# Performance work log

Hardware: AMD Instinct MI355X
Metric: run time of the kernel (lower is better)

The kernel has to match this reference:

```python
import jax, jax.numpy as jnp
import numpy as np

N = 100000      # nodes
E = 1600000     # edges
G = 8           # graphs in batch
H = 128         # hidden_dim
CNN = 768
MORPH = 6
NC = 5
EPS = 1e-5      # BatchNorm eps


def setup_inputs() -> dict:
    key = jax.random.key(0)
    ks = jax.random.split(key, 32)
    D = CNN + MORPH

    def w(k, shape, fan_in):
        # kaiming_normal_ (relu): std = sqrt(2/fan_in)
        return jax.random.normal(k, shape, jnp.float32) * np.sqrt(2.0 / fan_in)

    inp = {
        "cnn_features": jax.random.normal(ks[0], (N, CNN), jnp.float32),
        "morph_features": jax.random.normal(ks[1], (N, MORPH), jnp.float32),
        "cell_edge_index": jax.random.randint(ks[2], (2, E), 0, N, jnp.int32),
        "batch": jnp.sort(jax.random.randint(ks[3], (N,), 0, G, jnp.int32)),
        # GCN layers (weights stored [in, out])
        "gcn1_w": w(ks[4], (D, H), D), "gcn1_b": jnp.zeros((H,), jnp.float32),
        "gcn2_w": w(ks[5], (H, H), H), "gcn2_b": jnp.zeros((H,), jnp.float32),
        "gcn3_w": w(ks[6], (H, H), H), "gcn3_b": jnp.zeros((H,), jnp.float32),
        # BatchNorm affine params (eval mode, running_mean=0 running_var=1)
        "bn1_g": jnp.ones((H,), jnp.float32), "bn1_b": jnp.zeros((H,), jnp.float32),
        "bn2_g": jnp.ones((H,), jnp.float32), "bn2_b": jnp.zeros((H,), jnp.float32),
        "bn3_g": jnp.ones((H,), jnp.float32), "bn3_b": jnp.zeros((H,), jnp.float32),
        # attention gate: Linear(H,H) -> tanh -> Linear(H,1)
        "att_w1": w(ks[7], (H, H), H), "att_b1": jnp.zeros((H,), jnp.float32),
        "att_w2": w(ks[8], (H, 1), H), "att_b2": jnp.zeros((1,), jnp.float32),
        # classifier MLP
        "cls_w1": w(ks[9], (H, 2 * H), H), "cls_b1": jnp.zeros((2 * H,), jnp.float32),
        "cbn1_g": jnp.ones((2 * H,), jnp.float32), "cbn1_b": jnp.zeros((2 * H,), jnp.float32),
        "cls_w2": w(ks[10], (2 * H, H), 2 * H), "cls_b2": jnp.zeros((H,), jnp.float32),
        "cbn2_g": jnp.ones((H,), jnp.float32), "cbn2_b": jnp.zeros((H,), jnp.float32),
        "cls_w3": w(ks[11], (H, NC), H), "cls_b3": jnp.zeros((NC,), jnp.float32),
    }
    return inp


def _bn_eval(x, gamma, beta):
    # BatchNorm1d eval: running_mean=0, running_var=1
    return x * (gamma / np.sqrt(1.0 + EPS)) + beta


def _gcn(x, w, b, src, dst, dinv):
    h = x @ w                                   # [N, out]
    norm = dinv[src] * dinv[dst]                # [E]
    msg = h[src] * norm[:, None]                # [E, out]
    agg = jax.ops.segment_sum(msg, dst, num_segments=N)
    agg = agg + h * (dinv * dinv)[:, None]      # self-loop contribution
    return agg + b


def _forward(cnn_features, morph_features,
             gcn1_w, gcn1_b, gcn2_w, gcn2_b, gcn3_w, gcn3_b,
             bn1_g, bn1_b, bn2_g, bn2_b, bn3_g, bn3_b,
             att_w1, att_b1, att_w2, att_b2,
             cls_w1, cls_b1, cbn1_g, cbn1_b,
             cls_w2, cls_b2, cbn2_g, cbn2_b,
             cls_w3, cls_b3,
             cell_edge_index, batch):
    x = jnp.concatenate([cnn_features, morph_features], axis=1)  # [N, 774]
    src, dst = cell_edge_index[0], cell_edge_index[1]
    # symmetric GCN normalization with self-loops: deg = in-degree + 1
    deg = jax.ops.segment_sum(jnp.ones((E,), x.dtype), dst, num_segments=N) + 1.0
    dinv = jax.lax.rsqrt(deg)

    x1 = jax.nn.relu(_bn_eval(_gcn(x, gcn1_w, gcn1_b, src, dst, dinv), bn1_g, bn1_b))
    x2 = jax.nn.relu(_bn_eval(_gcn(x1, gcn2_w, gcn2_b, src, dst, dinv), bn2_g, bn2_b))
    x3 = jax.nn.relu(_bn_eval(_gcn(x2, gcn3_w, gcn3_b, src, dst, dinv), bn3_g, bn3_b))
    x_out = x1 + x2 + x3                                        # [N, H]

    # GlobalAttention pooling: segment softmax over per-graph nodes
    gate = jnp.tanh(x_out @ att_w1 + att_b1) @ att_w2 + att_b2  # [N, 1]
    gate = gate[:, 0]
    gmax = jax.ops.segment_max(gate, batch, num_segments=G)
    a = jnp.exp(gate - gmax[batch])
    denom = jax.ops.segment_sum(a, batch, num_segments=G)
    alpha = a / denom[batch]
    pooled = jax.ops.segment_sum(alpha[:, None] * x_out, batch, num_segments=G)  # [G, H]

    # classifier (dropout off, BN eval)
    h = jax.nn.relu(_bn_eval(pooled @ cls_w1 + cls_b1, cbn1_g, cbn1_b))
    h = jax.nn.relu(_bn_eval(h @ cls_w2 + cls_b2, cbn2_g, cbn2_b))
    return h @ cls_w3 + cls_b3                                  # [G, NC]


def reference(cnn_features, morph_features, cell_edge_index, batch,
              gcn1_w, gcn1_b, gcn2_w, gcn2_b, gcn3_w, gcn3_b,
              bn1_g, bn1_b, bn2_g, bn2_b, bn3_g, bn3_b,
              att_w1, att_b1, att_w2, att_b2,
              cls_w1, cls_b1, cbn1_g, cbn1_b,
              cls_w2, cls_b2, cbn2_g, cbn2_b,
              cls_w3, cls_b3):
    return _forward(cnn_features, morph_features,
                    gcn1_w, gcn1_b, gcn2_w, gcn2_b, gcn3_w, gcn3_b,
                    bn1_g, bn1_b, bn2_g, bn2_b, bn3_g, bn3_b,
                    att_w1, att_b1, att_w2, att_b2,
                    cls_w1, cls_b1, cbn1_g, cbn1_b,
                    cls_w2, cls_b2, cbn2_g, cbn2_b,
                    cls_w3, cls_b3,
                    cell_edge_index, batch)
```

## Files before the change

### kernel.cpp

```cpp
#include <hip/hip_runtime.h>
#include <hip/hip_bf16.h>

#define EPSV 1e-5f

typedef short short8v __attribute__((ext_vector_type(8)));
typedef float f32x4 __attribute__((ext_vector_type(4)));

__device__ __forceinline__ unsigned short f2bf(float f){
  unsigned u = __float_as_uint(f);
  unsigned r = u + 0x7fffu + ((u >> 16) & 1u);
  return (unsigned short)(r >> 16);
}
__device__ __forceinline__ unsigned pk2bf(float x, float y){
  return (unsigned)f2bf(x) | ((unsigned)f2bf(y) << 16);
}
__device__ __forceinline__ float bf2f(unsigned short s){
  return __uint_as_float(((unsigned)s) << 16);
}
__device__ __forceinline__ float bflo(unsigned u){ return __uint_as_float(u << 16); }
__device__ __forceinline__ float bfhi(unsigned u){ return __uint_as_float(u & 0xffff0000u); }

__global__ void hist_kernel(const int* __restrict__ dst, int* __restrict__ deg, int E){
  int i = blockIdx.x*256 + threadIdx.x;
  if (i < E) atomicAdd(&deg[dst[i]], 1);
}

__global__ void scan_partial(const int* __restrict__ deg, int* __restrict__ bsums, int N){
  __shared__ int sd[256];
  int t = threadIdx.x;
  int base = blockIdx.x*1024 + t*4;
  int s = 0;
  if (base+0 < N) s += deg[base+0];
  if (base+1 < N) s += deg[base+1];
  if (base+2 < N) s += deg[base+2];
  if (base+3 < N) s += deg[base+3];
  sd[t]=s; __syncthreads();
  for (int off=128; off>0; off>>=1){
    if (t<off) sd[t]+=sd[t+off];
    __syncthreads();
  }
  if (t==0) bsums[blockIdx.x]=sd[0];
}

__global__ void scan_bsums(int* bsums, int* row_start, int B, int N, int E){
  if (threadIdx.x==0 && blockIdx.x==0){
    int run=0;
    for (int b=0;b<B;b++){ int v=bsums[b]; bsums[b]=run; run+=v; }
    row_start[N]=E;
  }
}

__global__ void scan_final(const int* __restrict__ deg, const int* __restrict__ bsums,
                           int* __restrict__ row_start, int* __restrict__ cursor,
                           float* __restrict__ dinv, int N){
  __shared__ int sd[256];
  int t=threadIdx.x, b=blockIdx.x;
  int base=b*1024+t*4;
  int v0=0,v1=0,v2=0,v3=0;
  if (base+0<N) v0=deg[base+0];
  if (base+1<N) v1=deg[base+1];
  if (base+2<N) v2=deg[base+2];
  if (base+3<N) v3=deg[base+3];
  int s=v0+v1+v2+v3;
  sd[t]=s; __syncthreads();
  for (int off=1; off<256; off<<=1){
    int x = (t>=off)?sd[t-off]:0;
    __syncthreads();
    sd[t]+=x;
    __syncthreads();
  }
  int excl = sd[t]-s + bsums[b];
  int e0=excl, e1=excl+v0, e2=e1+v1, e3=e2+v2;
  if (base+0<N){ row_start[base+0]=e0; cursor[base+0]=e0; dinv[base+0]=rsqrtf((float)v0+1.0f); }
  if (base+1<N){ row_start[base+1]=e1; cursor[base+1]=e1; dinv[base+1]=rsqrtf((float)v1+1.0f); }
  if (base+2<N){ row_start[base+2]=e2; cursor[base+2]=e2; dinv[base+2]=rsqrtf((float)v2+1.0f); }
  if (base+3<N){ row_start[base+3]=e3; cursor[base+3]=e3; dinv[base+3]=rsqrtf((float)v3+1.0f); }
}

__global__ void scatter_kernel(const int* __restrict__ src, const int* __restrict__ dst,
                               int* __restrict__ cursor, int* __restrict__ csr_src, int E){
  int i = blockIdx.x*256 + threadIdx.x;
  if (i < E){
    int d = dst[i];
    int pos = atomicAdd(&cursor[d], 1);
    csr_src[pos] = src[i];
  }
}

__global__ void wsplit_kernel(const float* __restrict__ W, unsigned short* __restrict__ WT,
                              int D, int Dpad){
  int k = blockIdx.x*256 + threadIdx.x;
  int c = blockIdx.y;
  if (k >= Dpad) return;
  float v = (k < D) ? W[(size_t)k*128 + c] : 0.f;
  WT[(size_t)c*Dpad + k] = f2bf(v);
}

__global__ void wsplit_all(const float* __restrict__ W2, const float* __restrict__ W3,
                           const float* __restrict__ WA,
                           unsigned short* __restrict__ w2T, unsigned short* __restrict__ w3T,
                           unsigned short* __restrict__ aT_hi, unsigned short* __restrict__ aT_lo){
  int k = threadIdx.x;
  int c = blockIdx.y;
  int z = blockIdx.z;
  if (z == 0){
    w2T[c*128 + k] = f2bf(W2[(size_t)k*128 + c]);
  } else if (z == 1){
    w3T[c*128 + k] = f2bf(W3[(size_t)k*128 + c]);
  } else {
    float v = WA[(size_t)k*128 + c];
    unsigned short h = f2bf(v);
    aT_hi[c*128 + k] = h;
    aT_lo[c*128 + k] = f2bf(v - bf2f(h));
  }
}

#define LOADA(KC) { \
  const int gk0 = (KC) + akseg; \
  if ((Rst < N) && (gk0 + 32 <= Da)){ \
    const float4* p4 = (const float4*)(xa + (size_t)Rst*Da + gk0); \
    pa0=p4[0]; pa1=p4[1]; pa2=p4[2]; pa3=p4[3]; pa4=p4[4]; pa5=p4[5]; pa6=p4[6]; pa7=p4[7]; \
  } else { \
    float tmp[32]; \
    _Pragma("unroll") \
    for (int q=0;q<32;q++){ \
      int gk = gk0 + q; float x = 0.f; \
      if (Rst < N){ \
        if (gk < Da) x = xa[(size_t)Rst*Da + gk]; \
        else if (gk < D) x = xb[(size_t)Rst*Db + (gk - Da)]; \
      } \
      tmp[q]=x; } \
    pa0=*(float4*)&tmp[0];  pa1=*(float4*)&tmp[4];  pa2=*(float4*)&tmp[8];  pa3=*(float4*)&tmp[12]; \
    pa4=*(float4*)&tmp[16]; pa5=*(float4*)&tmp[20]; pa6=*(float4*)&tmp[24]; pa7=*(float4*)&tmp[28]; \
  } }

#define LOADW(KC) { \
  const unsigned short* ph = wrowp + (KC); \
  pw0=*(const uint4*)(ph); pw1=*(const uint4*)(ph+8); pw2=*(const uint4*)(ph+16); pw3=*(const uint4*)(ph+24); }

__global__ __launch_bounds__(256, 3) void gemm_mfma_kernel(
    const float* __restrict__ xa, const float* __restrict__ xb,
    const unsigned short* __restrict__ WT,
    unsigned short* __restrict__ outb, int N, int Da, int Db, int Dpad)
{
  __shared__ unsigned short Abf[128*64];
  __shared__ unsigned short Bbf[128*64];

  const int tid  = threadIdx.x;
  const int lane = tid & 63;
  const int wave = tid >> 6;
  const int lr   = lane & 15;
  const int kg   = lane >> 4;
  const int rowBase = blockIdx.x * 128;
  const int D = Da + Db;

  f32x4 acc[2][8];
  #pragma unroll
  for (int s=0;s<2;s++)
    #pragma unroll
    for (int c=0;c<8;c++){ acc[s][c][0]=0.f; acc[s][c][1]=0.f; acc[s][c][2]=0.f; acc[s][c][3]=0.f; }

  const int arow = tid >> 1;
  const int akseg = (tid & 1) * 32;
  const int Rst = rowBase + arow;
  const int abase = arow*128 + akseg*2;
  const int aswz  = (arow & 7) << 4;
  const unsigned short* wrowp = WT + (size_t)arow*Dpad + akseg;

  float4 pa0,pa1,pa2,pa3,pa4,pa5,pa6,pa7;
  uint4  pw0,pw1,pw2,pw3;

  LOADA(0)
  LOADW(0)

  for (int kc = 0; kc < Dpad; kc += 64){
    __syncthreads();
    {
      unsigned u[4];
      u[0]=pk2bf(pa0.x,pa0.y); u[1]=pk2bf(pa0.z,pa0.w); u[2]=pk2bf(pa1.x,pa1.y); u[3]=pk2bf(pa1.z,pa1.w);
      *(uint4*)((char*)Abf + ((abase+ 0)^aswz)) = *(const uint4*)u;
      u[0]=pk2bf(pa2.x,pa2.y); u[1]=pk2bf(pa2.z,pa2.w); u[2]=pk2bf(pa3.x,pa3.y); u[3]=pk2bf(pa3.z,pa3.w);
      *(uint4*)((char*)Abf + ((abase+16)^aswz)) = *(const uint4*)u;
      u[0]=pk2bf(pa4.x,pa4.y); u[1]=pk2bf(pa4.z,pa4.w); u[2]=pk2bf(pa5.x,pa5.y); u[3]=pk2bf(pa5.z,pa5.w);
      *(uint4*)((char*)Abf + ((abase+32)^aswz)) = *(const uint4*)u;
      u[0]=pk2bf(pa6.x,pa6.y); u[1]=pk2bf(pa6.z,pa6.w); u[2]=pk2bf(pa7.x,pa7.y); u[3]=pk2bf(pa7.z,pa7.w);
      *(uint4*)((char*)Abf + ((abase+48)^aswz)) = *(const uint4*)u;
      *(uint4*)((char*)Bbf + ((abase+ 0)^aswz)) = pw0;
      *(uint4*)((char*)Bbf + ((abase+16)^aswz)) = pw1;
      *(uint4*)((char*)Bbf + ((abase+32)^aswz)) = pw2;
      *(uint4*)((char*)Bbf + ((abase+48)^aswz)) = pw3;
    }
    __syncthreads();
    const int kn = kc + 64;
    if (kn < Dpad){
      LOADA(kn)
      LOADW(kn)
    }
    #pragma unroll
    for (int ks=0; ks<2; ks++){
      const int kb = ks*64 + kg*16;
      const int r0 = wave*32 + lr;
      const int r1 = r0 + 16;
      const int offA0 = (r0*128 + kb) ^ ((r0&7)<<4);
      const int offA1 = (r1*128 + kb) ^ ((r1&7)<<4);
      short8v a0 = *(const short8v*)((const char*)Abf + offA0);
      short8v a1 = *(const short8v*)((const char*)Abf + offA1);
      #pragma unroll
      for (int ct=0; ct<8; ct++){
        const int c = ct*16 + lr;
        const int offB = (c*128 + kb) ^ ((c&7)<<4);
        short8v b = *(const short8v*)((const char*)Bbf + offB);
        acc[0][ct] = __builtin_amdgcn_mfma_f32_16x16x32_bf16(a0, b, acc[0][ct], 0,0,0);
        acc[1][ct] = __builtin_amdgcn_mfma_f32_16x16x32_bf16(a1, b, acc[1][ct], 0,0,0);
      }
    }
  }
  const int wrow = rowBase + wave*32;
  #pragma unroll
  for (int strip=0; strip<2; strip++){
    #pragma unroll
    for (int ct=0; ct<8; ct++){
      #pragma unroll
      for (int i=0;i<4;i++){
        int R = wrow + strip*16 + kg*4 + i;
        int C = ct*16 + lr;
        if (R < N) outb[(size_t)R*128 + C] = f2bf(acc[strip][ct][i]);
      }
    }
  }
}

__global__ __launch_bounds__(256, 3) void gemm_bf16_kernel(
    const unsigned short* __restrict__ xa,
    const unsigned short* __restrict__ WT,
    unsigned short* __restrict__ outb, int N)
{
  __shared__ unsigned short Abf[128*64];
  __shared__ unsigned short Bbf[128*64];

  const int tid  = threadIdx.x;
  const int lane = tid & 63;
  const int wave = tid >> 6;
  const int lr   = lane & 15;
  const int kg   = lane >> 4;
  const int rowBase = blockIdx.x * 128;

  f32x4 acc[2][8];
  #pragma unroll
  for (int s=0;s<2;s++)
    #pragma unroll
    for (int c=0;c<8;c++){ acc[s][c][0]=0.f; acc[s][c][1]=0.f; acc[s][c][2]=0.f; acc[s][c][3]=0.f; }

  const int arow = tid >> 1;
  const int akseg = (tid & 1) * 32;
  const int Rst = rowBase + arow;
  const int abase = arow*128 + akseg*2;
  const int aswz  = (arow & 7) << 4;
  const unsigned short* arp = xa + (size_t)Rst*128 + akseg;
  const unsigned short* wrp = WT + (size_t)arow*128 + akseg;

  uint4 pa0,pa1,pa2,pa3, pw0,pw1,pw2,pw3;
  uint4 z4; z4.x=0; z4.y=0; z4.z=0; z4.w=0;
  if (Rst < N){ pa0=*(const uint4*)(arp); pa1=*(const uint4*)(arp+8); pa2=*(const uint4*)(arp+16); pa3=*(const uint4*)(arp+24); }
  else { pa0=z4; pa1=z4; pa2=z4; pa3=z4; }
  pw0=*(const uint4*)(wrp); pw1=*(const uint4*)(wrp+8); pw2=*(const uint4*)(wrp+16); pw3=*(const uint4*)(wrp+24);

  #pragma unroll
  for (int kc = 0; kc < 128; kc += 64){
    __syncthreads();
    *(uint4*)((char*)Abf + ((abase+ 0)^aswz)) = pa0;
    *(uint4*)((char*)Abf + ((abase+16)^aswz)) = pa1;
    *(uint4*)((char*)Abf + ((abase+32)^aswz)) = pa2;
    *(uint4*)((char*)Abf + ((abase+48)^aswz)) = pa3;
    *(uint4*)((char*)Bbf + ((abase+ 0)^aswz)) = pw0;
    *(uint4*)((char*)Bbf + ((abase+16)^aswz)) = pw1;
    *(uint4*)((char*)Bbf + ((abase+32)^aswz)) = pw2;
    *(uint4*)((char*)Bbf + ((abase+48)^aswz)) = pw3;
    __syncthreads();
    if (kc == 0){
      if (Rst < N){ pa0=*(const uint4*)(arp+64); pa1=*(const uint4*)(arp+72); pa2=*(const uint4*)(arp+80); pa3=*(const uint4*)(arp+88); }
      pw0=*(const uint4*)(wrp+64); pw1=*(const uint4*)(wrp+72); pw2=*(const uint4*)(wrp+80); pw3=*(const uint4*)(wrp+88);
    }
    #pragma unroll
    for (int ks=0; ks<2; ks++){
      const int kb = ks*64 + kg*16;
      const int r0 = wave*32 + lr;
      const int r1 = r0 + 16;
      const int offA0 = (r0*128 + kb) ^ ((r0&7)<<4);
      const int offA1 = (r1*128 + kb) ^ ((r1&7)<<4);
      short8v a0 = *(const short8v*)((const char*)Abf + offA0);
      short8v a1 = *(const short8v*)((const char*)Abf + offA1);
      #pragma unroll
      for (int ct=0; ct<8; ct++){
        const int c = ct*16 + lr;
        const int offB = (c*128 + kb) ^ ((c&7)<<4);
        short8v b = *(const short8v*)((const char*)Bbf + offB);
        acc[0][ct] = __builtin_amdgcn_mfma_f32_16x16x32_bf16(a0, b, acc[0][ct], 0,0,0);
        acc[1][ct] = __builtin_amdgcn_mfma_f32_16x16x32_bf16(a1, b, acc[1][ct], 0,0,0);
      }
    }
  }
  const int wrow = rowBase + wave*32;
  #pragma unroll
  for (int strip=0; strip<2; strip++){
    #pragma unroll
    for (int ct=0; ct<8; ct++){
      #pragma unroll
      for (int i=0;i<4;i++){
        int R = wrow + strip*16 + kg*4 + i;
        int C = ct*16 + lr;
        if (R < N) outb[(size_t)R*128 + C] = f2bf(acc[strip][ct][i]);
      }
    }
  }
}

__global__ __launch_bounds__(256) void att_pool_kernel(
    const unsigned short* __restrict__ xa,
    const unsigned short* __restrict__ WhiT, const unsigned short* __restrict__ WloT,
    const float* __restrict__ b1, const float* __restrict__ w2, const float* __restrict__ b2,
    const int* __restrict__ batch,
    float* __restrict__ pooled, float* __restrict__ denom, int N)
{
  __shared__ unsigned short Abf[128*64];
  __shared__ unsigned short Bhi[128*64];
  __shared__ unsigned short Blo[128*64];
  __shared__ float sden[8];
  __shared__ float sAex[128];
  __shared__ int   sBatch[128];

  const int tid  = threadIdx.x;
  const int lane = tid & 63;
  const int wave = tid >> 6;
  const int lr   = lane & 15;
  const int kg   = lane >> 4;
  const int rowBase = blockIdx.x * 128;

  if (tid < 8) sden[tid] = 0.f;
  if (tid < 128){
    int R = rowBase + tid;
    sBatch[tid] = (R < N) ? batch[R] : -1;
  }

  f32x4 acc[2][8];
  #pragma unroll
  for (int s=0;s<2;s++)
    #pragma unroll
    for (int c=0;c<8;c++){ acc[s][c][0]=0.f; acc[s][c][1]=0.f; acc[s][c][2]=0.f; acc[s][c][3]=0.f; }

  const int arow = tid >> 1;
  const int akseg = (tid & 1) * 32;
  const int Rst = rowBase + arow;
  const int abase = arow*128 + akseg*2;
  const int aswz  = (arow & 7) << 4;
  const unsigned short* arp = xa + (size_t)Rst*128 + akseg;

  #pragma unroll
  for (int kc = 0; kc < 128; kc += 64){
    __syncthreads();
    {
      uint4 z4; z4.x=0; z4.y=0; z4.z=0; z4.w=0;
      uint4 a0=z4,a1=z4,a2=z4,a3=z4;
      if (Rst < N){
        a0=*(const uint4*)(arp+kc); a1=*(const uint4*)(arp+kc+8);
        a2=*(const uint4*)(arp+kc+16); a3=*(const uint4*)(arp+kc+24);
      }
      *(uint4*)((char*)Abf + ((abase+ 0)^aswz)) = a0;
      *(uint4*)((char*)Abf + ((abase+16)^aswz)) = a1;
      *(uint4*)((char*)Abf + ((abase+32)^aswz)) = a2;
      *(uint4*)((char*)Abf + ((abase+48)^aswz)) = a3;
      const unsigned short* ph = WhiT + (size_t)arow*128 + kc + akseg;
      const unsigned short* pl = WloT + (size_t)arow*128 + kc + akseg;
      *(uint4*)((char*)Bhi + ((abase+ 0)^aswz)) = *(const uint4*)(ph);
      *(uint4*)((char*)Bhi + ((abase+16)^aswz)) = *(const uint4*)(ph+8);
      *(uint4*)((char*)Bhi + ((abase+32)^aswz)) = *(const uint4*)(ph+16);
      *(uint4*)((char*)Bhi + ((abase+48)^aswz)) = *(const uint4*)(ph+24);
      *(uint4*)((char*)Blo + ((abase+ 0)^aswz)) = *(const uint4*)(pl);
      *(uint4*)((char*)Blo + ((abase+16)^aswz)) = *(const uint4*)(pl+8);
      *(uint4*)((char*)Blo + ((abase+32)^aswz)) = *(const uint4*)(pl+16);
      *(uint4*)((char*)Blo + ((abase+48)^aswz)) = *(const uint4*)(pl+24);
    }
    __syncthreads();
    #pragma unroll
    for (int ks=0; ks<2; ks++){
      const int kb = ks*64 + kg*16;
      const int r0 = wave*32 + lr;
      const int r1 = r0 + 16;
      const int offA0 = (r0*128 + kb) ^ ((r0&7)<<4);
      const int offA1 = (r1*128 + kb) ^ ((r1&7)<<4);
      short8v a0 = *(const short8v*)((const char*)Abf + offA0);
      short8v a1 = *(const short8v*)((const char*)Abf + offA1);
      #pragma unroll
      for (int ct=0; ct<8; ct++){
        const int c = ct*16 + lr;
        const int offB = (c*128 + kb) ^ ((c&7)<<4);
        short8v bh = *(const short8v*)((const char*)Bhi + offB);
        short8v bl = *(const short8v*)((const char*)Blo + offB);
        acc[0][ct] = __builtin_amdgcn_mfma_f32_16x16x32_bf16(a0, bh, acc[0][ct], 0,0,0);
        acc[0][ct] = __builtin_amdgcn_mfma_f32_16x16x32_bf16(a0, bl, acc[0][ct], 0,0,0);
        acc[1][ct] = __builtin_amdgcn_mfma_f32_16x16x32_bf16(a1, bh, acc[1][ct], 0,0,0);
        acc[1][ct] = __builtin_amdgcn_mfma_f32_16x16x32_bf16(a1, bl, acc[1][ct], 0,0,0);
      }
    }
  }
  float b1v[8], w2v[8];
  #pragma unroll
  for (int ct=0; ct<8; ct++){
    b1v[ct] = b1[ct*16 + lr];
    w2v[ct] = w2[ct*16 + lr];
  }
  const float bias2 = b2[0];
  #pragma unroll
  for (int strip=0; strip<2; strip++){
    #pragma unroll
    for (int i=0;i<4;i++){
      float p = 0.f;
      #pragma unroll
      for (int ct=0; ct<8; ct++){
        p += tanhf(acc[strip][ct][i] + b1v[ct]) * w2v[ct];
      }
      p += __shfl_xor(p, 1, 16);
      p += __shfl_xor(p, 2, 16);
      p += __shfl_xor(p, 4, 16);
      p += __shfl_xor(p, 8, 16);
      if (lr == 0){
        int rib = wave*32 + strip*16 + kg*4 + i;
        int R = rowBase + rib;
        if (R < N){
          float e = expf(p + bias2);
          sAex[rib] = e;
          atomicAdd(&sden[sBatch[rib]], e);
        }
      }
    }
  }
  __syncthreads();
  {
    const int cpair = tid & 63;
    const int rgrp  = tid >> 6;
    const unsigned* __restrict__ xu = (const unsigned*)xa;
    float p0 = 0.f, p1 = 0.f;
    int gcur = -1;
    for (int r = rgrp*32; r < rgrp*32 + 32; ++r){
      int R = rowBase + r;
      if (R >= N) break;
      int g = sBatch[r];
      if (g != gcur){
        if (gcur >= 0){
          atomicAdd(&pooled[gcur*128 + cpair*2],     p0);
          atomicAdd(&pooled[gcur*128 + cpair*2 + 1], p1);
        }
        p0 = 0.f; p1 = 0.f; gcur = g;
      }
      float e = sAex[r];
      unsigned u = xu[(size_t)R*64 + cpair];
      p0 = __builtin_fmaf(e, bflo(u), p0);
      p1 = __builtin_fmaf(e, bfhi(u), p1);
    }
    if (gcur >= 0){
      atomicAdd(&pooled[gcur*128 + cpair*2],     p0);
      atomicAdd(&pooled[gcur*128 + cpair*2 + 1], p1);
    }
  }
  if (tid < 8 && sden[tid] != 0.f) atomicAdd(&denom[tid], sden[tid]);
}

#define GFMA8(U, NJ) \
  a0=__builtin_fmaf(bflo(U.x),(NJ),a0); a1=__builtin_fmaf(bfhi(U.x),(NJ),a1); \
  a2=__builtin_fmaf(bflo(U.y),(NJ),a2); a3=__builtin_fmaf(bfhi(U.y),(NJ),a3); \
  a4=__builtin_fmaf(bflo(U.z),(NJ),a4); a5=__builtin_fmaf(bfhi(U.z),(NJ),a5); \
  a6=__builtin_fmaf(bflo(U.w),(NJ),a6); a7=__builtin_fmaf(bfhi(U.w),(NJ),a7);

__global__ __launch_bounds__(256) void gather_kernel(
    const unsigned short* __restrict__ hb, const float* __restrict__ dinv,
    const int* __restrict__ row_start, const int* __restrict__ csr_src,
    const float* __restrict__ bias, const float* __restrict__ bng, const float* __restrict__ bnb,
    const unsigned short* __restrict__ x1in, const unsigned short* __restrict__ x2in,
    unsigned short* __restrict__ out, int N, int mode)
{
  const int grp = (blockIdx.x * 256 + threadIdx.x) >> 4;
  const int sl  = threadIdx.x & 15;
  if (grp >= N) return;
  const int i = grp;
  const float di = dinv[i];
  const uint4* __restrict__ h4 = (const uint4*)hb;

  float a0,a1,a2,a3,a4,a5,a6,a7;
  {
    uint4 u = h4[(size_t)i*16 + sl];
    float w0 = di*di;
    a0=bflo(u.x)*w0; a1=bfhi(u.x)*w0; a2=bflo(u.y)*w0; a3=bfhi(u.y)*w0;
    a4=bflo(u.z)*w0; a5=bfhi(u.z)*w0; a6=bflo(u.w)*w0; a7=bfhi(u.w)*w0;
  }
  int base = row_start[i];
  const int s1 = row_start[i+1];
  while (base + 16 <= s1){
    int sv = csr_src[base + sl];
    float nv = dinv[sv]*di;
    #pragma unroll
    for (int j=0; j<16; j+=4){
      int sj0 = __shfl(sv, j,   16);
      int sj1 = __shfl(sv, j+1, 16);
      int sj2 = __shfl(sv, j+2, 16);
      int sj3 = __shfl(sv, j+3, 16);
      float nj0 = __shfl(nv, j,   16);
      float nj1 = __shfl(nv, j+1, 16);
      float nj2 = __shfl(nv, j+2, 16);
      float nj3 = __shfl(nv, j+3, 16);
      uint4 u0 = h4[(size_t)sj0*16 + sl];
      uint4 u1 = h4[(size_t)sj1*16 + sl];
      uint4 u2 = h4[(size_t)sj2*16 + sl];
      uint4 u3 = h4[(size_t)sj3*16 + sl];
      GFMA8(u0, nj0)
      GFMA8(u1, nj1)
      GFMA8(u2, nj2)
      GFMA8(u3, nj3)
    }
    base += 16;
  }
  const int rem = s1 - base;
  if (rem > 0){
    int sv = 0; float nv = 0.f;
    if (sl < rem){ sv = csr_src[base + sl]; nv = dinv[sv]*di; }
    for (int j=0; j<rem; j++){
      int   sj = __shfl(sv, j, 16);
      float nj = __shfl(nv, j, 16);
      uint4 u = h4[(size_t)sj*16 + sl];
      GFMA8(u, nj)
    }
  }
  const int f0 = sl*8;
  const float bsc = rsqrtf(1.0f + EPSV);
  float4 bi0 = *(const float4*)(bias + f0);
  float4 bi1 = *(const float4*)(bias + f0 + 4);
  float4 g0 = *(const float4*)(bng + f0);
  float4 g1 = *(const float4*)(bng + f0 + 4);
  float4 be0 = *(const float4*)(bnb + f0);
  float4 be1 = *(const float4*)(bnb + f0 + 4);
  float v[8];
  v[0] = fmaxf(0.f, (a0+bi0.x)*(g0.x*bsc) + be0.x);
  v[1] = fmaxf(0.f, (a1+bi0.y)*(g0.y*bsc) + be0.y);
  v[2] = fmaxf(0.f, (a2+bi0.z)*(g0.z*bsc) + be0.z);
  v[3] = fmaxf(0.f, (a3+bi0.w)*(g0.w*bsc) + be0.w);
  v[4] = fmaxf(0.f, (a4+bi1.x)*(g1.x*bsc) + be1.x);
  v[5] = fmaxf(0.f, (a5+bi1.y)*(g1.y*bsc) + be1.y);
  v[6] = fmaxf(0.f, (a6+bi1.z)*(g1.z*bsc) + be1.z);
  v[7] = fmaxf(0.f, (a7+bi1.w)*(g1.w*bsc) + be1.w);
  if (mode == 2){
    uint4 up = ((const uint4*)x1in)[(size_t)i*16 + sl];
    uint4 uq = ((const uint4*)x2in)[(size_t)i*16 + sl];
    v[0]+=bflo(up.x)+bflo(uq.x); v[1]+=bfhi(up.x)+bfhi(uq.x);
    v[2]+=bflo(up.y)+bflo(uq.y); v[3]+=bfhi(up.y)+bfhi(uq.y);
    v[4]+=bflo(up.z)+bflo(uq.z); v[5]+=bfhi(up.z)+bfhi(uq.z);
    v[6]+=bflo(up.w)+bflo(uq.w); v[7]+=bfhi(up.w)+bfhi(uq.w);
  }
  unsigned o[4];
  o[0]=pk2bf(v[0],v[1]); o[1]=pk2bf(v[2],v[3]); o[2]=pk2bf(v[4],v[5]); o[3]=pk2bf(v[6],v[7]);
  ((uint4*)out)[(size_t)i*16 + sl] = *(const uint4*)o;
}

__global__ __launch_bounds__(256) void classifier_kernel(
    const float* __restrict__ pooled, const float* __restrict__ denom,
    const float* __restrict__ w1, const float* __restrict__ b1,
    const float* __restrict__ g1, const float* __restrict__ be1,
    const float* __restrict__ w2, const float* __restrict__ b2,
    const float* __restrict__ g2, const float* __restrict__ be2,
    const float* __restrict__ w3, const float* __restrict__ b3,
    float* __restrict__ outp)
{
  __shared__ float pl[8*128];
  __shared__ float h1[8*256];
  __shared__ float h2l[8*128];
  int t = threadIdx.x;
  for (int idx = t; idx < 1024; idx += 256){
    int g = idx >> 7;
    pl[idx] = pooled[idx] / denom[g];
  }
  __syncthreads();
  {
    float a0=0,a1=0,a2=0,a3=0,a4=0,a5=0,a6=0,a7=0;
    for (int k=0; k<128; k++){
      float w = w1[k*256 + t];
      a0 = __builtin_fmaf(pl[0*128+k], w, a0);
      a1 = __builtin_fmaf(pl[1*128+k], w, a1);
      a2 = __builtin_fmaf(pl[2*128+k], w, a2);
      a3 = __builtin_fmaf(pl[3*128+k], w, a3);
      a4 = __builtin_fmaf(pl[4*128+k], w, a4);
      a5 = __builtin_fmaf(pl[5*128+k], w, a5);
      a6 = __builtin_fmaf(pl[6*128+k], w, a6);
      a7 = __builtin_fmaf(pl[7*128+k], w, a7);
    }
    float s = g1[t]*rsqrtf(1.0f + EPSV);
    float bb = b1[t], tb = be1[t];
    h1[0*256+t] = fmaxf(0.f, (a0+bb)*s + tb);
    h1[1*256+t] = fmaxf(0.f, (a1+bb)*s + tb);
    h1[2*256+t] = fmaxf(0.f, (a2+bb)*s + tb);
    h1[3*256+t] = fmaxf(0.f, (a3+bb)*s + tb);
    h1[4*256+t] = fmaxf(0.f, (a4+bb)*s + tb);
    h1[5*256+t] = fmaxf(0.f, (a5+bb)*s + tb);
    h1[6*256+t] = fmaxf(0.f, (a6+bb)*s + tb);
    h1[7*256+t] = fmaxf(0.f, (a7+bb)*s + tb);
  }
  __syncthreads();
  if (t < 128){
    float a0=0,a1=0,a2=0,a3=0,a4=0,a5=0,a6=0,a7=0;
    for (int k=0; k<256; k++){
      float w = w2[k*128 + t];
      a0 = __builtin_fmaf(h1[0*256+k], w, a0);
      a1 = __builtin_fmaf(h1[1*256+k], w, a1);
      a2 = __builtin_fmaf(h1[2*256+k], w, a2);
      a3 = __builtin_fmaf(h1[3*256+k], w, a3);
      a4 = __builtin_fmaf(h1[4*256+k], w, a4);
      a5 = __builtin_fmaf(h1[5*256+k], w, a5);
      a6 = __builtin_fmaf(h1[6*256+k], w, a6);
      a7 = __builtin_fmaf(h1[7*256+k], w, a7);
    }
    float s = g2[t]*rsqrtf(1.0f + EPSV);
    float bb = b2[t], tb = be2[t];
    h2l[0*128+t] = fmaxf(0.f, (a0+bb)*s + tb);
    h2l[1*128+t] = fmaxf(0.f, (a1+bb)*s + tb);
    h2l[2*128+t] = fmaxf(0.f, (a2+bb)*s + tb);
    h2l[3*128+t] = fmaxf(0.f, (a3+bb)*s + tb);
    h2l[4*128+t] = fmaxf(0.f, (a4+bb)*s + tb);
    h2l[5*128+t] = fmaxf(0.f, (a5+bb)*s + tb);
    h2l[6*128+t] = fmaxf(0.f, (a6+bb)*s + tb);
    h2l[7*128+t] = fmaxf(0.f, (a7+bb)*s + tb);
  }
  __syncthreads();
  if (t < 40){
    int g = t/5, c = t%5;
    float s = 0.f;
    for (int k=0; k<128; k++) s = __builtin_fmaf(h2l[g*128+k], w3[k*5+c], s);
    outp[t] = s + b3[c];
  }
}

extern "C" void kernel_launch(void* const* d_in, const int* in_sizes, int n_in,
                              void* d_out, int out_size, void* d_ws, size_t ws_size,
                              hipStream_t stream)
{
  const float* cnn   = (const float*)d_in[0];
  const float* morph = (const float*)d_in[1];
  const int*   eidx  = (const int*)d_in[2];
  const int*   batch = (const int*)d_in[3];
  const float* g1w = (const float*)d_in[4];
  const float* g1b = (const float*)d_in[5];
  const float* g2w = (const float*)d_in[6];
  const float* g2b = (const float*)d_in[7];
  const float* g3w = (const float*)d_in[8];
  const float* g3b = (const float*)d_in[9];
  const float* bn1g=(const float*)d_in[10], *bn1b=(const float*)d_in[11];
  const float* bn2g=(const float*)d_in[12], *bn2b=(const float*)d_in[13];
  const float* bn3g=(const float*)d_in[14], *bn3b=(const float*)d_in[15];
  const float* aw1=(const float*)d_in[16], *ab1=(const float*)d_in[17];
  const float* aw2=(const float*)d_in[18], *ab2=(const float*)d_in[19];
  const float* cw1=(const float*)d_in[20], *cb1=(const float*)d_in[21];
  const float* c1g=(const float*)d_in[22], *c1b=(const float*)d_in[23];
  const float* cw2=(const float*)d_in[24], *cb2=(const float*)d_in[25];
  const float* c2g=(const float*)d_in[26], *c2b=(const float*)d_in[27];
  const float* cw3=(const float*)d_in[28], *cb3=(const float*)d_in[29];

  const int N = in_sizes[3];
  const int E = in_sizes[2] / 2;
  const int CNNW = in_sizes[0] / N;
  const int MOR  = in_sizes[1] / N;
  const int D = CNNW + MOR;
  const int Dpad1 = ((D + 63)/64)*64;

  char* p = (char*)d_ws;
  auto alloc = [&](size_t bytes)->char* {
    char* r = p; p += (bytes + 255) & ~(size_t)255; return r;
  };
  unsigned short* hbuf = (unsigned short*)alloc((size_t)N*128*2);
  unsigned short* x1   = (unsigned short*)alloc((size_t)N*128*2);
  unsigned short* x2   = (unsigned short*)alloc((size_t)N*128*2);
  float* dinv  = (float*)alloc((size_t)N*4);
  char* zstart = p;
  int* deg      = (int*)alloc((size_t)N*4);
  float* denom  = (float*)alloc(8*4);
  float* pooled = (float*)alloc(8*128*4);
  size_t zbytes = (size_t)(p - zstart);
  int* row_start=(int*)alloc((size_t)(N+1)*4);
  int* cursor  = (int*)alloc((size_t)N*4);
  int* csr_src = (int*)alloc((size_t)E*4);
  int* bsums   = (int*)alloc(4096);
  unsigned short* w1T = (unsigned short*)alloc((size_t)128*Dpad1*2);
  unsigned short* w2T = (unsigned short*)alloc((size_t)128*128*2);
  unsigned short* w3T = (unsigned short*)alloc((size_t)128*128*2);
  unsigned short* aw1hiT = (unsigned short*)alloc((size_t)128*128*2);
  unsigned short* aw1loT = (unsigned short*)alloc((size_t)128*128*2);

  hipMemsetAsync(zstart, 0, zbytes, stream);

  const int* srcp = eidx;
  const int* dstp = eidx + E;

  int gE = (E + 255)/256;
  int B  = (N + 1023)/1024;
  int gMfma = (N + 127)/128;
  int gGat  = (N + 15)/16;

  hist_kernel<<<dim3(gE), dim3(256), 0, stream>>>(dstp, deg, E);
  scan_partial<<<dim3(B), dim3(256), 0, stream>>>(deg, bsums, N);
  scan_bsums<<<dim3(1), dim3(64), 0, stream>>>(bsums, row_start, B, N, E);
  scan_final<<<dim3(B), dim3(256), 0, stream>>>(deg, bsums, row_start, cursor, dinv, N);
  scatter_kernel<<<dim3(gE), dim3(256), 0, stream>>>(srcp, dstp, cursor, csr_src, E);

  wsplit_kernel<<<dim3((Dpad1+255)/256, 128), dim3(256), 0, stream>>>(g1w, w1T, D, Dpad1);
  wsplit_all<<<dim3(1, 128, 3), dim3(128), 0, stream>>>(g2w, g3w, aw1, w2T, w3T, aw1hiT, aw1loT);

  gemm_mfma_kernel<<<dim3(gMfma), dim3(256), 0, stream>>>(cnn, morph, w1T, hbuf, N, CNNW, MOR, Dpad1);
  gather_kernel<<<dim3(gGat), dim3(256), 0, stream>>>(hbuf, dinv, row_start, csr_src,
      g1b, bn1g, bn1b, (const unsigned short*)nullptr, (const unsigned short*)nullptr, x1, N, 0);
  gemm_bf16_kernel<<<dim3(gMfma), dim3(256), 0, stream>>>(x1, w2T, hbuf, N);
  gather_kernel<<<dim3(gGat), dim3(256), 0, stream>>>(hbuf, dinv, row_start, csr_src,
      g2b, bn2g, bn2b, (const unsigned short*)nullptr, (const unsigned short*)nullptr, x2, N, 0);
  gemm_bf16_kernel<<<dim3(gMfma), dim3(256), 0, stream>>>(x2, w3T, hbuf, N);
  gather_kernel<<<dim3(gGat), dim3(256), 0, stream>>>(hbuf, dinv, row_start, csr_src,
      g3b, bn3g, bn3b, x1, x2, x1, N, 2);

  att_pool_kernel<<<dim3(gMfma), dim3(256), 0, stream>>>(x1, aw1hiT, aw1loT,
      ab1, aw2, ab2, batch, pooled, denom, N);

  classifier_kernel<<<dim3(1), dim3(256), 0, stream>>>(pooled, denom,
      cw1, cb1, c1g, c1b, cw2, cb2, c2g, c2b, cw3, cb3, (float*)d_out);
}
```

Measured before the change: 725.8 us.

## Sort gather rows by degree bucket and batch remainder neighbor loads

Adds a degree histogram, scan and scatter pass that builds a permutation of nodes grouped by in-degree bucket. The gather kernel then processes nodes in that order, so 16-lane groups sharing a wavefront have similar trip counts and less divergence. The remainder loop now issues up to four neighbor row loads before the FMAs, with masked weights, to raise memory-level parallelism. The cost is three extra small kernels with global atomics, an indirection through perm, and loss of the contiguous output-row locality the sequential order had.

```diff
diff --git a/kernel.cpp b/kernel.cpp
--- a/kernel.cpp
+++ b/kernel.cpp
@@ -84,6 +84,37 @@
     int d = dst[i];
     int pos = atomicAdd(&cursor[d], 1);
     csr_src[pos] = src[i];
+  }
+}
+
+__global__ void deghist_kernel(const int* __restrict__ deg, int* __restrict__ dhist, int N){
+  __shared__ int sb[64];
+  int t = threadIdx.x;
+  if (t < 64) sb[t] = 0;
+  __syncthreads();
+  int i = blockIdx.x*256 + t;
+  if (i < N){
+    int b = deg[i]; if (b > 63) b = 63;
+    atomicAdd(&sb[b], 1);
+  }
+  __syncthreads();
+  if (t < 64 && sb[t] != 0) atomicAdd(&dhist[t], sb[t]);
+}
+
+__global__ void degscan_kernel(const int* __restrict__ dhist, int* __restrict__ dcur){
+  if (threadIdx.x == 0 && blockIdx.x == 0){
+    int run = 0;
+    for (int b=0;b<64;b++){ int v = dhist[b]; dcur[b] = run; run += v; }
+  }
+}
+
+__global__ void degscatter_kernel(const int* __restrict__ deg, int* __restrict__ dcur,
+                                  int* __restrict__ perm, int N){
+  int i = blockIdx.x*256 + threadIdx.x;
+  if (i < N){
+    int b = deg[i]; if (b > 63) b = 63;
+    int pos = atomicAdd(&dcur[b], 1);
+    perm[pos] = i;
   }
 }
 
@@ -474,6 +505,7 @@
 __global__ __launch_bounds__(256) void gather_kernel(
     const unsigned short* __restrict__ hb, const float* __restrict__ dinv,
     const int* __restrict__ row_start, const int* __restrict__ csr_src,
+    const int* __restrict__ perm,
     const float* __restrict__ bias, const float* __restrict__ bng, const float* __restrict__ bnb,
     const unsigned short* __restrict__ x1in, const unsigned short* __restrict__ x2in,
     unsigned short* __restrict__ out, int N, int mode)
@@ -481,7 +513,7 @@
   const int grp = (blockIdx.x * 256 + threadIdx.x) >> 4;
   const int sl  = threadIdx.x & 15;
   if (grp >= N) return;
-  const int i = grp;
+  const int i = perm[grp];
   const float di = dinv[i];
   const uint4* __restrict__ h4 = (const uint4*)hb;
 
@@ -522,11 +554,20 @@
   if (rem > 0){
     int sv = 0; float nv = 0.f;
     if (sl < rem){ sv = csr_src[base + sl]; nv = dinv[sv]*di; }
-    for (int j=0; j<rem; j++){
-      int   sj = __shfl(sv, j, 16);
-      float nj = __shfl(nv, j, 16);
-      uint4 u = h4[(size_t)sj*16 + sl];
-      GFMA8(u, nj)
+    for (int j0=0; j0<rem; j0+=4){
+      uint4 u[4]; float njv[4];
+      #pragma unroll
+      for (int q=0;q<4;q++){
+        const int j = j0 + q;
+        const int jj = (j < rem) ? j : 0;
+        int   sjq = __shfl(sv, jj, 16);
+        float njq = __shfl(nv, jj, 16);
+        if (j >= rem) njq = 0.f;
+        u[q] = h4[(size_t)sjq*16 + sl];
+        njv[q] = njq;
+      }
+      #pragma unroll
+      for (int q=0;q<4;q++){ GFMA8(u[q], njv[q]) }
     }
   }
   const int f0 = sl*8;
@@ -679,10 +720,13 @@
   int* deg      = (int*)alloc((size_t)N*4);
   float* denom  = (float*)alloc(8*4);
   float* pooled = (float*)alloc(8*128*4);
+  int* dhist    = (int*)alloc(64*4);
+  int* dcur     = (int*)alloc(64*4);
   size_t zbytes = (size_t)(p - zstart);
   int* row_start=(int*)alloc((size_t)(N+1)*4);
   int* cursor  = (int*)alloc((size_t)N*4);
   int* csr_src = (int*)alloc((size_t)E*4);
+  int* perm    = (int*)alloc((size_t)N*4);
   int* bsums   = (int*)alloc(4096);
   unsigned short* w1T = (unsigned short*)alloc((size_t)128*Dpad1*2);
   unsigned short* w2T = (unsigned short*)alloc((size_t)128*128*2);
@@ -696,6 +740,7 @@
   const int* dstp = eidx + E;
 
   int gE = (E + 255)/256;
+  int gN = (N + 255)/256;
   int B  = (N + 1023)/1024;
   int gMfma = (N + 127)/128;
   int gGat  = (N + 15)/16;
@@ -706,17 +751,21 @@
   scan_final<<<dim3(B), dim3(256), 0, stream>>>(deg, bsums, row_start, cursor, dinv, N);
   scatter_kernel<<<dim3(gE), dim3(256), 0, stream>>>(srcp, dstp, cursor, csr_src, E);
 
+  deghist_kernel<<<dim3(gN), dim3(256), 0, stream>>>(deg, dhist, N);
+  degscan_kernel<<<dim3(1), dim3(64), 0, stream>>>(dhist, dcur);
+  degscatter_kernel<<<dim3(gN), dim3(256), 0, stream>>>(deg, dcur, perm, N);
+
   wsplit_kernel<<<dim3((Dpad1+255)/256, 128), dim3(256), 0, stream>>>(g1w, w1T, D, Dpad1);
   wsplit_all<<<dim3(1, 128, 3), dim3(128), 0, stream>>>(g2w, g3w, aw1, w2T, w3T, aw1hiT, aw1loT);
 
   gemm_mfma_kernel<<<dim3(gMfma), dim3(256), 0, stream>>>(cnn, morph, w1T, hbuf, N, CNNW, MOR, Dpad1);
-  gather_kernel<<<dim3(gGat), dim3(256), 0, stream>>>(hbuf, dinv, row_start, csr_src,
+  gather_kernel<<<dim3(gGat), dim3(256), 0, stream>>>(hbuf, dinv, row_start, csr_src, perm,
       g1b, bn1g, bn1b, (const unsigned short*)nullptr, (const unsigned short*)nullptr, x1, N, 0);
   gemm_bf16_kernel<<<dim3(gMfma), dim3(256), 0, stream>>>(x1, w2T, hbuf, N);
-  gather_kernel<<<dim3(gGat), dim3(256), 0, stream>>>(hbuf, dinv, row_start, csr_src,
+  gather_kernel<<<dim3(gGat), dim3(256), 0, stream>>>(hbuf, dinv, row_start, csr_src, perm,
       g2b, bn2g, bn2b, (const unsigned short*)nullptr, (const unsigned short*)nullptr, x2, N, 0);
   gemm_bf16_kernel<<<dim3(gMfma), dim3(256), 0, stream>>>(x2, w3T, hbuf, N);
-  gather_kernel<<<dim3(gGat), dim3(256), 0, stream>>>(hbuf, dinv, row_start, csr_src,
+  gather_kernel<<<dim3(gGat), dim3(256), 0, stream>>>(hbuf, dinv, row_start, csr_src, perm,
       g3b, bn3g, bn3b, x1, x2, x1, N, 2);
 
   att_pool_kernel<<<dim3(gMfma), dim3(256), 0, stream>>>(x1, aw1hiT, aw1loT,
```

After: 996.6 us. 1.37x slower.

## Precompute per-edge normalization weights in CSR and batch tail gathers

Applied to the files above, without the earlier changes.

The scatter kernel now stores each CSR entry as an (src, dinv[dst]*dinv[src]) pair, so the three gather kernels no longer do a dependent random dinv[src] lookup per edge. The remainder loop in the gather now issues four neighbor row loads before the FMAs, giving more memory-level parallelism on the tail edges. In exchange the CSR array doubles in size, so each gather streams more index bytes and the scatter kernel does extra random dinv reads once.

```diff
diff --git a/kernel.cpp b/kernel.cpp
--- a/kernel.cpp
+++ b/kernel.cpp
@@ -78,12 +78,15 @@
 }
 
 __global__ void scatter_kernel(const int* __restrict__ src, const int* __restrict__ dst,
-                               int* __restrict__ cursor, int* __restrict__ csr_src, int E){
+                               int* __restrict__ cursor, const float* __restrict__ dinv,
+                               int2* __restrict__ csr_ew, int E){
   int i = blockIdx.x*256 + threadIdx.x;
   if (i < E){
+    int s = src[i];
     int d = dst[i];
     int pos = atomicAdd(&cursor[d], 1);
-    csr_src[pos] = src[i];
+    float w = dinv[d]*dinv[s];
+    csr_ew[pos] = make_int2(s, __float_as_int(w));
   }
 }
 
@@ -473,7 +476,7 @@
 
 __global__ __launch_bounds__(256) void gather_kernel(
     const unsigned short* __restrict__ hb, const float* __restrict__ dinv,
-    const int* __restrict__ row_start, const int* __restrict__ csr_src,
+    const int* __restrict__ row_start, const int2* __restrict__ csr_ew,
     const float* __restrict__ bias, const float* __restrict__ bng, const float* __restrict__ bnb,
     const unsigned short* __restrict__ x1in, const unsigned short* __restrict__ x2in,
     unsigned short* __restrict__ out, int N, int mode)
@@ -495,8 +498,9 @@
   int base = row_start[i];
   const int s1 = row_start[i+1];
   while (base + 16 <= s1){
-    int sv = csr_src[base + sl];
-    float nv = dinv[sv]*di;
+    int2 ew = csr_ew[base + sl];
+    int sv = ew.x;
+    float nv = __int_as_float(ew.y);
     #pragma unroll
     for (int j=0; j<16; j+=4){
       int sj0 = __shfl(sv, j,   16);
@@ -521,12 +525,25 @@
   const int rem = s1 - base;
   if (rem > 0){
     int sv = 0; float nv = 0.f;
-    if (sl < rem){ sv = csr_src[base + sl]; nv = dinv[sv]*di; }
-    for (int j=0; j<rem; j++){
-      int   sj = __shfl(sv, j, 16);
-      float nj = __shfl(nv, j, 16);
-      uint4 u = h4[(size_t)sj*16 + sl];
-      GFMA8(u, nj)
+    if (sl < rem){
+      int2 ew = csr_ew[base + sl];
+      sv = ew.x;
+      nv = __int_as_float(ew.y);
+    }
+    for (int j0=0; j0<rem; j0+=4){
+      uint4 u[4]; float njv[4];
+      #pragma unroll
+      for (int q=0;q<4;q++){
+        const int j = j0 + q;
+        const int jj = (j < rem) ? j : 0;
+        int   sjq = __shfl(sv, jj, 16);
+        float njq = __shfl(nv, jj, 16);
+        if (j >= rem) njq = 0.f;
+        u[q] = h4[(size_t)sjq*16 + sl];
+        njv[q] = njq;
+      }
+      #pragma unroll
+      for (int q=0;q<4;q++){ GFMA8(u[q], njv[q]) }
     }
   }
   const int f0 = sl*8;
@@ -682,7 +699,7 @@
   size_t zbytes = (size_t)(p - zstart);
   int* row_start=(int*)alloc((size_t)(N+1)*4);
   int* cursor  = (int*)alloc((size_t)N*4);
-  int* csr_src = (int*)alloc((size_t)E*4);
+  int2* csr_ew = (int2*)alloc((size_t)E*8);
   int* bsums   = (int*)alloc(4096);
   unsigned short* w1T = (unsigned short*)alloc((size_t)128*Dpad1*2);
   unsigned short* w2T = (unsigned short*)alloc((size_t)128*128*2);
@@ -704,19 +721,19 @@
   scan_partial<<<dim3(B), dim3(256), 0, stream>>>(deg, bsums, N);
   scan_bsums<<<dim3(1), dim3(64), 0, stream>>>(bsums, row_start, B, N, E);
   scan_final<<<dim3(B), dim3(256), 0, stream>>>(deg, bsums, row_start, cursor, dinv, N);
-  scatter_kernel<<<dim3(gE), dim3(256), 0, stream>>>(srcp, dstp, cursor, csr_src, E);
+  scatter_kernel<<<dim3(gE), dim3(256), 0, stream>>>(srcp, dstp, cursor, dinv, csr_ew, E);
 
   wsplit_kernel<<<dim3((Dpad1+255)/256, 128), dim3(256), 0, stream>>>(g1w, w1T, D, Dpad1);
   wsplit_all<<<dim3(1, 128, 3), dim3(128), 0, stream>>>(g2w, g3w, aw1, w2T, w3T, aw1hiT, aw1loT);
 
   gemm_mfma_kernel<<<dim3(gMfma), dim3(256), 0, stream>>>(cnn, morph, w1T, hbuf, N, CNNW, MOR, Dpad1);
-  gather_kernel<<<dim3(gGat), dim3(256), 0, stream>>>(hbuf, dinv, row_start, csr_src,
+  gather_kernel<<<dim3(gGat), dim3(256), 0, stream>>>(hbuf, dinv, row_start, csr_ew,
       g1b, bn1g, bn1b, (const unsigned short*)nullptr, (const unsigned short*)nullptr, x1, N, 0);
   gemm_bf16_kernel<<<dim3(gMfma), dim3(256), 0, stream>>>(x1, w2T, hbuf, N);
-  gather_kernel<<<dim3(gGat), dim3(256), 0, stream>>>(hbuf, dinv, row_start, csr_src,
+  gather_kernel<<<dim3(gGat), dim3(256), 0, stream>>>(hbuf, dinv, row_start, csr_ew,
       g2b, bn2g, bn2b, (const unsigned short*)nullptr, (const unsigned short*)nullptr, x2, N, 0);
   gemm_bf16_kernel<<<dim3(gMfma), dim3(256), 0, stream>>>(x2, w3T, hbuf, N);
-  gather_kernel<<<dim3(gGat), dim3(256), 0, stream>>>(hbuf, dinv, row_start, csr_src,
+  gather_kernel<<<dim3(gGat), dim3(256), 0, stream>>>(hbuf, dinv, row_start, csr_ew,
       g3b, bn3g, bn3b, x1, x2, x1, N, 2);
 
   att_pool_kernel<<<dim3(gMfma), dim3(256), 0, stream>>>(x1, aw1hiT, aw1loT,
```

Measured after the change: 678.3 us. 6.5% less time.
